# Performance work log

Measured on AMD Instinct MI355X. Metric: run time of the kernel, lower is better.

## Reference

```python
import jax, jax.numpy as jnp
import numpy as np

B, A_IN, C_IN, H, W_ = 8, 16, 4, 64, 64   # batch, input atoms, input capsules, spatial
K, C_OUT, A_OUT, ROUTINGS = 5, 8, 32, 3
EPS = 1e-7


def setup_inputs() -> dict:
    key = jax.random.key(0)
    k1, k2 = jax.random.split(key)
    x = jax.random.normal(k1, (B, A_IN, C_IN, H, W_), dtype=jnp.float32)
    # kaiming_uniform_(fan_in, relu): bound = sqrt(3) * sqrt(2) / sqrt(fan_in)
    fan_in = A_IN * K * K
    bound = float(np.sqrt(6.0 / fan_in))
    W = jax.random.uniform(k2, (C_OUT * A_OUT, A_IN, K, K), jnp.float32, -bound, bound)
    b = jnp.full((1, 1, C_OUT, A_OUT), 0.1, dtype=jnp.float32)
    return {"x": x, "W": W, "b": b}


def _squash(v):
    # v: (..., atoms); SegCaps squash with epsilon inside sqrt
    sq = jnp.sum(v * v, axis=-1, keepdims=True)
    return v * (sq / (1.0 + sq) / jnp.sqrt(sq + EPS))


def reference(x, W, b):
    # Faithful to torch: permute then raw row-major reshapes (byte reinterpret)
    t = jnp.transpose(x, (2, 0, 3, 4, 1))                      # (C_IN, B, H, W, A_IN)
    t = t.reshape(C_IN * B, H, W_, A_IN).reshape(-1, A_IN, H, W_)
    conv = jax.lax.conv_general_dilated(
        t, W, window_strides=(1, 1), padding="SAME",
        dimension_numbers=("NCHW", "OIHW", "NCHW"))             # (C_IN*B, C_OUT*A_OUT, h, w)
    ch, cw = conv.shape[2], conv.shape[3]
    votes = conv.reshape(B, C_IN, ch, cw, C_OUT, A_OUT)         # raw reinterpret, as in torch
    biases = jnp.tile(b, (ch, cw, 1, 1))                        # (h, w, C_OUT, A_OUT)

    # dynamic routing (SegCaps update_routing)
    logits = jnp.zeros((B, C_IN, ch, cw, C_OUT), dtype=votes.dtype)
    activation = None
    for _ in range(ROUTINGS):
        route = jax.nn.softmax(logits, axis=-1)                 # (B, Cin, h, w, Cout)
        preact = jnp.einsum("bihwo,bihwoa->bhwoa", route, votes) + biases
        activation = _squash(preact)                            # (B, h, w, Cout, A)
        agreement = jnp.einsum("bihwoa,bhwoa->bihwo", votes, activation)
        logits = logits + agreement
    return jnp.transpose(activation, (0, 4, 3, 1, 2))           # (B, A_OUT, C_OUT, h, w)
```

## Files before the change

kernel.cpp:

```cpp
#include <hip/hip_runtime.h>
#include <hip/hip_bf16.h>


typedef _Float16 half8 __attribute__((ext_vector_type(8)));
typedef _Float16 half4v __attribute__((ext_vector_type(4)));
typedef float floatx4 __attribute__((ext_vector_type(4)));

#define EPSF 1e-7f

__global__ __launch_bounds__(256) void k_prep(const float* __restrict__ x,
                                              const float* __restrict__ W,
                                              _Float16* __restrict__ th,
                                              _Float16* __restrict__ Wp) {
  const int tid = threadIdx.x;
  if (blockIdx.x < 256) {
    __shared__ float lin[32 * 306 + 18];
    const int bid = blockIdx.x;
    const int n   = bid >> 3;
    const int a0h = (bid >> 2) & 1;
    const int W0  = (bid & 3) * 16;
    const int ci = n >> 3, b0 = n & 7;
    const float* xb = x + b0 * 262144 + ci * 4096 + W0;
    for (int p = 0; p < 8; ++p) {
      int rr = p * 64 + (tid >> 2);
      int qq = (tid & 3) * 4;
      int a1 = rr >> 5, m = rr & 31;
      float4 v = *(const float4*)(xb + a1 * 16384 + (a0h * 32 + m) * 64 + qq);
      float* d = lin + m * 306 + a1 * 18 + qq;
      d[0] = v.x; d[1] = v.y; d[2] = v.z; d[3] = v.w;
    }
    __syncthreads();
    _Float16* tb = th + (size_t)n * 65536 + a0h * 32768 + W0 * 128;
    for (int hh = 0; hh < 4; ++hh) {
      int w1 = tid >> 4, a1 = tid & 15;
      half8 v;
#pragma unroll
      for (int j = 0; j < 8; ++j)
        v[j] = (_Float16)lin[(j * 4 + hh) * 306 + a1 * 18 + w1];
      *(half8*)(tb + hh * 8192 + w1 * 128 + a1 * 8) = v;
    }
  } else {
    int id = (blockIdx.x - 256) * 256 + tid;
    int a  = id & 15;
    int oc = (id >> 4) & 255;
    int kk = id >> 12;
    Wp[id] = (kk < 25) ? (_Float16)W[oc * 400 + a * 25 + kk] : (_Float16)0.0f;
  }
}

__global__ __launch_bounds__(256) void k_conv(const _Float16* __restrict__ th,
                                              const _Float16* __restrict__ Wp,
                                              _Float16* __restrict__ votes) {
  __shared__ _Float16 slab[6528];
  const int y2 = blockIdx.x;
  const int n  = blockIdx.y;
  const int y0 = y2 * 2;
  const int tid = threadIdx.x;

  for (int c = tid; c < 816; c += 256) {
    int ah  = c / 408;
    int rem = c - ah * 408;
    int rr  = rem / 68;
    int cc  = rem - rr * 68;
    int row = y0 + rr - 2;
    int col = cc - 2;
    half8 v = {};
    if (row >= 0 && row < 64 && col >= 0 && col < 64)
      v = *(const half8*)(th + (size_t)(((n * 2 + ah) * 64 + row) * 64 + col) * 8);
    *(half8*)(slab + c * 8) = v;
  }
  __syncthreads();

  const int lane  = tid & 63;
  const int wv    = tid >> 6;
  const int col16 = lane & 15;
  const int quad  = lane >> 4;
  const int t     = quad >> 1;
  const int a0h   = quad & 1;
  const int m0    = wv * 64;

  floatx4 acc[2][4][4] = {};

  const _Float16* wbase = Wp + (size_t)t * 4096 + (m0 + col16) * 16 + a0h * 8;
  half8 af[4], an[4];
#pragma unroll
  for (int oct = 0; oct < 4; ++oct)
    af[oct] = *(const half8*)(wbase + oct * 256);

  for (int s = 0; s < 13; ++s) {
    int kkb = 2 * s + t; if (kkb > 24) kkb = 24;
    int ky = kkb / 5;
    int kx = kkb - ky * 5;
    const _Float16* lb = slab + a0h * 3264 + ky * 544 + (col16 + kx) * 8;
    half8 bf[2][4];
#pragma unroll
    for (int yy = 0; yy < 2; ++yy)
#pragma unroll
      for (int xt = 0; xt < 4; ++xt)
        bf[yy][xt] = *(const half8*)(lb + yy * 544 + xt * 128);
    int sn = (s + 1 < 13) ? s + 1 : s;
#pragma unroll
    for (int oct = 0; oct < 4; ++oct)
      an[oct] = *(const half8*)(wbase + (size_t)sn * 8192 + oct * 256);
#pragma unroll
    for (int oct = 0; oct < 4; ++oct)
#pragma unroll
      for (int yy = 0; yy < 2; ++yy)
#pragma unroll
        for (int xt = 0; xt < 4; ++xt)
          acc[yy][oct][xt] = __builtin_amdgcn_mfma_f32_16x16x32_f16(
              af[oct], bf[yy][xt], acc[yy][oct][xt], 0, 0, 0);
#pragma unroll
    for (int oct = 0; oct < 4; ++oct) af[oct] = an[oct];
  }

#pragma unroll
  for (int yy = 0; yy < 2; ++yy) {
    _Float16* vbase = votes + (size_t)n * 1048576 + (y0 + yy) * 64;
#pragma unroll
    for (int oct = 0; oct < 4; ++oct)
#pragma unroll
      for (int xt = 0; xt < 4; ++xt)
#pragma unroll
        for (int r = 0; r < 4; ++r) {
          int oc = m0 + oct * 16 + quad * 4 + r;
          int xx = xt * 16 + col16;
          vbase[(size_t)oc * 4096 + xx] = (_Float16)acc[yy][oct][xt][r];
        }
  }
}

__global__ __launch_bounds__(256) void k_routing2(
    const _Float16* __restrict__ votes, const float* __restrict__ bias,
    float* __restrict__ out) {
  __shared__ float so[256 * 36];
  const int tid  = threadIdx.x;
  const int lane = tid & 63;
  const int wv   = tid >> 6;
  const int bid  = blockIdx.x;
  const int bv = bid >> 7;
  const int h  = (bid >> 1) & 63;
  const int W0 = (bid & 1) * 32;

  float4 bia = *(const float4*)(bias + lane * 4);
  const int o  = lane >> 3;
  const int a0 = (lane & 7) * 4;

  for (int k = 0; k < 8; ++k) {
    const int wl = wv * 8 + k;
    const int w  = W0 + wl;
    const _Float16* vb = votes + (size_t)bv * 4194304 + h * 16384 + w * 256 + lane * 4;
    float4 v[4];
#pragma unroll
    for (int i = 0; i < 4; ++i) {
      half4v hv = *(const half4v*)(vb + (size_t)i * 1048576);
      v[i] = make_float4((float)hv.x, (float)hv.y, (float)hv.z, (float)hv.w);
    }

    float logit[4] = {0.f, 0.f, 0.f, 0.f};
    float act[4];

#pragma unroll
    for (int r = 0; r < 3; ++r) {
      float route[4];
#pragma unroll
      for (int i = 0; i < 4; ++i) {
        float m = logit[i];
        m = fmaxf(m, __shfl_xor(m, 8, 64));
        m = fmaxf(m, __shfl_xor(m, 16, 64));
        m = fmaxf(m, __shfl_xor(m, 32, 64));
        float e = __expf(logit[i] - m);
        float s = e;
        s += __shfl_xor(s, 8, 64);
        s += __shfl_xor(s, 16, 64);
        s += __shfl_xor(s, 32, 64);
        route[i] = e / s;
      }
      float pr[4] = {bia.x, bia.y, bia.z, bia.w};
#pragma unroll
      for (int i = 0; i < 4; ++i) {
        pr[0] = fmaf(route[i], v[i].x, pr[0]);
        pr[1] = fmaf(route[i], v[i].y, pr[1]);
        pr[2] = fmaf(route[i], v[i].z, pr[2]);
        pr[3] = fmaf(route[i], v[i].w, pr[3]);
      }
      float sq = pr[0]*pr[0] + pr[1]*pr[1] + pr[2]*pr[2] + pr[3]*pr[3];
      sq += __shfl_xor(sq, 1, 64);
      sq += __shfl_xor(sq, 2, 64);
      sq += __shfl_xor(sq, 4, 64);
      float scale = sq / (1.f + sq) / sqrtf(sq + EPSF);
#pragma unroll
      for (int j = 0; j < 4; ++j) act[j] = pr[j] * scale;

      if (r < 2) {
#pragma unroll
        for (int i = 0; i < 4; ++i) {
          float ag = v[i].x*act[0] + v[i].y*act[1] + v[i].z*act[2] + v[i].w*act[3];
          ag += __shfl_xor(ag, 1, 64);
          ag += __shfl_xor(ag, 2, 64);
          ag += __shfl_xor(ag, 4, 64);
          logit[i] += ag;
        }
      }
    }

#pragma unroll
    for (int j = 0; j < 4; ++j)
      so[((a0 + j) * 8 + o) * 36 + wl] = act[j];
  }
  __syncthreads();

  float* ob = out + (size_t)bv * 1048576 + h * 64 + W0;
  for (int p = 0; p < 8; ++p) {
    int r  = p * 32 + (tid >> 3);
    int w0 = (tid & 7) * 4;
    float4 v = *(const float4*)(so + r * 36 + w0);
    *(float4*)(ob + (size_t)r * 4096 + w0) = v;
  }
}

extern "C" void kernel_launch(void* const* d_in, const int* in_sizes, int n_in,
                              void* d_out, int out_size, void* d_ws, size_t ws_size,
                              hipStream_t stream) {
  const float* x  = (const float*)d_in[0];
  const float* W  = (const float*)d_in[1];
  const float* b  = (const float*)d_in[2];
  float* out = (float*)d_out;

  _Float16* th    = (_Float16*)d_ws;
  _Float16* Wp    = th + 2097152;
  _Float16* votes = Wp + 106496;

  k_prep<<<672, 256, 0, stream>>>(x, W, th, Wp);
  k_conv<<<dim3(32, 32), 256, 0, stream>>>(th, Wp, votes);
  k_routing2<<<1024, 256, 0, stream>>>(votes, b, out);
}
```

Baseline: 151.4 us.

## Retile conv to one row per block with deeper prefetch; prefetch votes in routing

The conv kernel now computes one output row per block instead of two. This halves the accumulators and targets three blocks per CU, and it doubles the grid. Weight fragments are prefetched two steps ahead and LDS B-fragments one step ahead, with the weight loads issued before the barrier. The routing kernel prefetches the next pixel's votes and keeps all eight activations in registers. It then writes output through a smaller padded LDS tile in two phases. The goal is better latency hiding and occupancy, paid for with redundant halo loads and extra barriers.

```diff
diff --git a/kernel.cpp b/kernel.cpp
--- a/kernel.cpp
+++ b/kernel.cpp
@@ -48,28 +48,26 @@
   }
 }
 
-__global__ __launch_bounds__(256) void k_conv(const _Float16* __restrict__ th,
-                                              const _Float16* __restrict__ Wp,
-                                              _Float16* __restrict__ votes) {
-  __shared__ _Float16 slab[6528];
-  const int y2 = blockIdx.x;
-  const int n  = blockIdx.y;
-  const int y0 = y2 * 2;
+__global__ __launch_bounds__(256, 3) void k_conv(
+    const _Float16* __restrict__ th, const _Float16* __restrict__ Wp,
+    _Float16* __restrict__ votes) {
+  __shared__ _Float16 slab[5440];
+  const int y = blockIdx.x;
+  const int n = blockIdx.y;
   const int tid = threadIdx.x;
 
-  for (int c = tid; c < 816; c += 256) {
-    int ah  = c / 408;
-    int rem = c - ah * 408;
+  for (int c = tid; c < 680; c += 256) {
+    int ah  = c / 340;
+    int rem = c - ah * 340;
     int rr  = rem / 68;
     int cc  = rem - rr * 68;
-    int row = y0 + rr - 2;
+    int row = y + rr - 2;
     int col = cc - 2;
     half8 v = {};
     if (row >= 0 && row < 64 && col >= 0 && col < 64)
       v = *(const half8*)(th + (size_t)(((n * 2 + ah) * 64 + row) * 64 + col) * 8);
     *(half8*)(slab + c * 8) = v;
   }
-  __syncthreads();
 
   const int lane  = tid & 63;
   const int wv    = tid >> 6;
@@ -79,61 +77,67 @@
   const int a0h   = quad & 1;
   const int m0    = wv * 64;
 
-  floatx4 acc[2][4][4] = {};
-
-  const _Float16* wbase = Wp + (size_t)t * 4096 + (m0 + col16) * 16 + a0h * 8;
-  half8 af[4], an[4];
+  floatx4 acc[4][4] = {};
+
+  const _Float16* wb = Wp + (size_t)t * 4096 + (m0 + col16) * 16 + a0h * 8;
+  half8 af[4], a1[4], a2[4], bf[4], b1[4];
+#pragma unroll
+  for (int oct = 0; oct < 4; ++oct) {
+    af[oct] = *(const half8*)(wb + oct * 256);
+    a1[oct] = *(const half8*)(wb + 8192 + oct * 256);
+  }
+
+  __syncthreads();
+
+  {
+    int kkb = t;
+    int ky = kkb / 5, kx = kkb - ky * 5;
+    const _Float16* lb = slab + (a0h * 340 + ky * 68 + col16 + kx) * 8;
+#pragma unroll
+    for (int xt = 0; xt < 4; ++xt)
+      bf[xt] = *(const half8*)(lb + xt * 128);
+  }
+
+  for (int s = 0; s < 13; ++s) {
+    int s2 = (s + 2 < 13) ? s + 2 : 12;
+#pragma unroll
+    for (int oct = 0; oct < 4; ++oct)
+      a2[oct] = *(const half8*)(wb + (size_t)s2 * 8192 + oct * 256);
+    int kkb1 = 2 * (s + 1) + t; if (kkb1 > 24) kkb1 = 24;
+    int ky1 = kkb1 / 5, kx1 = kkb1 - ky1 * 5;
+    const _Float16* lb1 = slab + (a0h * 340 + ky1 * 68 + col16 + kx1) * 8;
+#pragma unroll
+    for (int xt = 0; xt < 4; ++xt)
+      b1[xt] = *(const half8*)(lb1 + xt * 128);
+#pragma unroll
+    for (int oct = 0; oct < 4; ++oct)
+#pragma unroll
+      for (int xt = 0; xt < 4; ++xt)
+        acc[oct][xt] = __builtin_amdgcn_mfma_f32_16x16x32_f16(
+            af[oct], bf[xt], acc[oct][xt], 0, 0, 0);
+#pragma unroll
+    for (int oct = 0; oct < 4; ++oct) { af[oct] = a1[oct]; a1[oct] = a2[oct]; }
+#pragma unroll
+    for (int xt = 0; xt < 4; ++xt) bf[xt] = b1[xt];
+  }
+
+  _Float16* vbase = votes + (size_t)n * 1048576 + y * 64;
 #pragma unroll
   for (int oct = 0; oct < 4; ++oct)
-    af[oct] = *(const half8*)(wbase + oct * 256);
-
-  for (int s = 0; s < 13; ++s) {
-    int kkb = 2 * s + t; if (kkb > 24) kkb = 24;
-    int ky = kkb / 5;
-    int kx = kkb - ky * 5;
-    const _Float16* lb = slab + a0h * 3264 + ky * 544 + (col16 + kx) * 8;
-    half8 bf[2][4];
-#pragma unroll
-    for (int yy = 0; yy < 2; ++yy)
-#pragma unroll
-      for (int xt = 0; xt < 4; ++xt)
-        bf[yy][xt] = *(const half8*)(lb + yy * 544 + xt * 128);
-    int sn = (s + 1 < 13) ? s + 1 : s;
-#pragma unroll
-    for (int oct = 0; oct < 4; ++oct)
-      an[oct] = *(const half8*)(wbase + (size_t)sn * 8192 + oct * 256);
-#pragma unroll
-    for (int oct = 0; oct < 4; ++oct)
-#pragma unroll
-      for (int yy = 0; yy < 2; ++yy)
-#pragma unroll
-        for (int xt = 0; xt < 4; ++xt)
-          acc[yy][oct][xt] = __builtin_amdgcn_mfma_f32_16x16x32_f16(
-              af[oct], bf[yy][xt], acc[yy][oct][xt], 0, 0, 0);
-#pragma unroll
-    for (int oct = 0; oct < 4; ++oct) af[oct] = an[oct];
-  }
-
-#pragma unroll
-  for (int yy = 0; yy < 2; ++yy) {
-    _Float16* vbase = votes + (size_t)n * 1048576 + (y0 + yy) * 64;
-#pragma unroll
-    for (int oct = 0; oct < 4; ++oct)
-#pragma unroll
-      for (int xt = 0; xt < 4; ++xt)
-#pragma unroll
-        for (int r = 0; r < 4; ++r) {
-          int oc = m0 + oct * 16 + quad * 4 + r;
-          int xx = xt * 16 + col16;
-          vbase[(size_t)oc * 4096 + xx] = (_Float16)acc[yy][oct][xt][r];
-        }
-  }
-}
-
-__global__ __launch_bounds__(256) void k_routing2(
+#pragma unroll
+    for (int xt = 0; xt < 4; ++xt)
+#pragma unroll
+      for (int r = 0; r < 4; ++r) {
+        int oc = m0 + oct * 16 + quad * 4 + r;
+        int xx = xt * 16 + col16;
+        vbase[(size_t)oc * 4096 + xx] = (_Float16)acc[oct][xt][r];
+      }
+}
+
+__global__ __launch_bounds__(256) void k_routing3(
     const _Float16* __restrict__ votes, const float* __restrict__ bias,
     float* __restrict__ out) {
-  __shared__ float so[256 * 36];
+  __shared__ float so[128 * 37];
   const int tid  = threadIdx.x;
   const int lane = tid & 63;
   const int wv   = tid >> 6;
@@ -143,33 +147,41 @@
   const int W0 = (bid & 1) * 32;
 
   float4 bia = *(const float4*)(bias + lane * 4);
-  const int o  = lane >> 3;
-  const int a0 = (lane & 7) * 4;
+  const int o = lane >> 3;
+  const int m = lane & 7;
+
+  float act[8][4];
+
+  const _Float16* vb0 = votes + (size_t)bv * 4194304 + h * 16384
+                        + (W0 + wv * 8) * 256 + lane * 4;
+  half4v vn[4];
+#pragma unroll
+  for (int i = 0; i < 4; ++i)
+    vn[i] = *(const half4v*)(vb0 + (size_t)i * 1048576);
 
   for (int k = 0; k < 8; ++k) {
-    const int wl = wv * 8 + k;
-    const int w  = W0 + wl;
-    const _Float16* vb = votes + (size_t)bv * 4194304 + h * 16384 + w * 256 + lane * 4;
     float4 v[4];
 #pragma unroll
-    for (int i = 0; i < 4; ++i) {
-      half4v hv = *(const half4v*)(vb + (size_t)i * 1048576);
-      v[i] = make_float4((float)hv.x, (float)hv.y, (float)hv.z, (float)hv.w);
+    for (int i = 0; i < 4; ++i)
+      v[i] = make_float4((float)vn[i].x, (float)vn[i].y,
+                         (float)vn[i].z, (float)vn[i].w);
+    if (k < 7) {
+#pragma unroll
+      for (int i = 0; i < 4; ++i)
+        vn[i] = *(const half4v*)(vb0 + (k + 1) * 256 + (size_t)i * 1048576);
     }
 
     float logit[4] = {0.f, 0.f, 0.f, 0.f};
-    float act[4];
-
 #pragma unroll
     for (int r = 0; r < 3; ++r) {
       float route[4];
 #pragma unroll
       for (int i = 0; i < 4; ++i) {
-        float m = logit[i];
-        m = fmaxf(m, __shfl_xor(m, 8, 64));
-        m = fmaxf(m, __shfl_xor(m, 16, 64));
-        m = fmaxf(m, __shfl_xor(m, 32, 64));
-        float e = __expf(logit[i] - m);
+        float mx = logit[i];
+        mx = fmaxf(mx, __shfl_xor(mx, 8, 64));
+        mx = fmaxf(mx, __shfl_xor(mx, 16, 64));
+        mx = fmaxf(mx, __shfl_xor(mx, 32, 64));
+        float e = __expf(logit[i] - mx);
         float s = e;
         s += __shfl_xor(s, 8, 64);
         s += __shfl_xor(s, 16, 64);
@@ -190,12 +202,13 @@
       sq += __shfl_xor(sq, 4, 64);
       float scale = sq / (1.f + sq) / sqrtf(sq + EPSF);
 #pragma unroll
-      for (int j = 0; j < 4; ++j) act[j] = pr[j] * scale;
+      for (int j = 0; j < 4; ++j) act[k][j] = pr[j] * scale;
 
       if (r < 2) {
 #pragma unroll
         for (int i = 0; i < 4; ++i) {
-          float ag = v[i].x*act[0] + v[i].y*act[1] + v[i].z*act[2] + v[i].w*act[3];
+          float ag = v[i].x*act[k][0] + v[i].y*act[k][1]
+                   + v[i].z*act[k][2] + v[i].w*act[k][3];
           ag += __shfl_xor(ag, 1, 64);
           ag += __shfl_xor(ag, 2, 64);
           ag += __shfl_xor(ag, 4, 64);
@@ -203,19 +216,29 @@
         }
       }
     }
-
-#pragma unroll
-    for (int j = 0; j < 4; ++j)
-      so[((a0 + j) * 8 + o) * 36 + wl] = act[j];
-  }
-  __syncthreads();
+  }
 
   float* ob = out + (size_t)bv * 1048576 + h * 64 + W0;
-  for (int p = 0; p < 8; ++p) {
-    int r  = p * 32 + (tid >> 3);
-    int w0 = (tid & 7) * 4;
-    float4 v = *(const float4*)(so + r * 36 + w0);
-    *(float4*)(ob + (size_t)r * 4096 + w0) = v;
+#pragma unroll
+  for (int ph = 0; ph < 2; ++ph) {
+    if (ph) __syncthreads();
+#pragma unroll
+    for (int k = 0; k < 8; ++k)
+#pragma unroll
+      for (int jj = 0; jj < 2; ++jj) {
+        int rc = m * 16 + jj * 8 + o;
+        so[rc * 37 + wv * 8 + k] = act[k][2 * ph + jj];
+      }
+    __syncthreads();
+    for (int p = 0; p < 4; ++p) {
+      int rc = p * 32 + (tid >> 3);
+      int mm = rc >> 4, jj = (rc >> 3) & 1, oo = rc & 7;
+      int rg = mm * 32 + (2 * ph + jj) * 8 + oo;
+      int w0 = (tid & 7) * 4;
+      const float* sp = so + rc * 37 + w0;
+      float4 val = make_float4(sp[0], sp[1], sp[2], sp[3]);
+      *(float4*)(ob + (size_t)rg * 4096 + w0) = val;
+    }
   }
 }
 
@@ -232,6 +255,6 @@
   _Float16* votes = Wp + 106496;
 
   k_prep<<<672, 256, 0, stream>>>(x, W, th, Wp);
-  k_conv<<<dim3(32, 32), 256, 0, stream>>>(th, Wp, votes);
-  k_routing2<<<1024, 256, 0, stream>>>(votes, b, out);
-}
+  k_conv<<<dim3(64, 32), 256, 0, stream>>>(th, Wp, votes);
+  k_routing3<<<1024, 256, 0, stream>>>(votes, b, out);
+}
```

Result: no change. 152.8 us (+1.0%).
